# Performance work log

Hardware: AMD Instinct MI355X
Metric: run time of the kernel (lower is better)

## Reference

```python
import jax, jax.numpy as jnp
import numpy as np

B, C, F, T = 4, 64, 257, 256
H, OUT = 256, 64

def setup_inputs() -> dict:
    key = jax.random.key(0)
    ks = jax.random.split(key, 7)
    w = lambda k, shape: jax.random.normal(k, shape, dtype=jnp.float32) * 0.05
    return {
        "x": jax.random.normal(ks[0], (B, C, F, T), dtype=jnp.float32),
        "W_ih": w(ks[1], (4 * H, C)),   # torch LSTM weight_ih_l0, gate order i,f,g,o
        "W_hh": w(ks[2], (4 * H, H)),   # weight_hh_l0
        "b_ih": w(ks[3], (4 * H,)),
        "b_hh": w(ks[4], (4 * H,)),
        "W_lin": w(ks[5], (OUT, H)),
        "b_lin": w(ks[6], (OUT,)),
    }

def _lstm(y, W_ih, W_hh, b_ih, b_hh):
    # y: (N, T, C) -> (N, T, H); PyTorch gate order i, f, g, o
    N, Tl, _ = y.shape
    Hd = W_hh.shape[1]
    # precompute input contributions for all timesteps in one big GEMM
    x_gates = jnp.einsum('ntc,gc->ntg', y, W_ih) + b_ih + b_hh  # (N, T, 4H)

    def step(carry, xg):
        h, c = carry
        g = xg + h @ W_hh.T  # (N, 4H)
        i, f, gg, o = jnp.split(g, 4, axis=-1)
        c = jax.nn.sigmoid(f) * c + jax.nn.sigmoid(i) * jnp.tanh(gg)
        h = jax.nn.sigmoid(o) * jnp.tanh(c)
        return (h, c), h

    h0 = jnp.zeros((N, Hd), y.dtype)
    _, hs = jax.lax.scan(step, (h0, h0), jnp.swapaxes(x_gates, 0, 1))  # (T, N, H)
    return jnp.swapaxes(hs, 0, 1)  # (N, T, H)

def reference(x, W_ih, W_hh, b_ih, b_hh, W_lin, b_lin):
    b, c, f, t = x.shape
    y = x.transpose(0, 2, 3, 1).reshape(b * f, t, c)  # (B*F, T, C)
    h = _lstm(y, W_ih, W_hh, b_ih, b_hh)              # (B*F, T, H)
    out = h @ W_lin.T + b_lin                          # (B*F, T, OUT)
    return out.reshape(b, f, t, -1).transpose(0, 3, 1, 2)  # (B, OUT, F, T)
```

## Files before the change

kernel.cpp:

```cpp
#include <hip/hip_runtime.h>

#define NSEQ 1028
#define TT   256
#define CC   64
#define HH   256
#define NKT  10
#define AROWB 656
#define SLABE 32768
#define LSTM_LDS (2*16*AROWB + 2*SLABE*2)
#define OUTP_LDS (128*264*2 + 64*264*2)

typedef unsigned short u16;
typedef float  f32x4 __attribute__((ext_vector_type(4)));
typedef __bf16 v8bf  __attribute__((ext_vector_type(8)));

__device__ __forceinline__ u16 f2bf(float f){
  unsigned u = __builtin_bit_cast(unsigned, f);
  u += 0x7FFFu + ((u >> 16) & 1u);
  return (u16)(u >> 16);
}
__device__ __forceinline__ float sigm(float x){
  float t = __builtin_amdgcn_exp2f(-1.4426950408889634f * x);
  return __builtin_amdgcn_rcpf(1.0f + t);
}
__device__ __forceinline__ float tanh_f(float x){
  float a = __builtin_fabsf(x);
  float t = __builtin_amdgcn_exp2f(-2.885390081777927f * a);
  float r = (1.0f - t) * __builtin_amdgcn_rcpf(1.0f + t);
  return __builtin_copysignf(r, x);
}
__device__ __forceinline__ void mfma_a(f32x4& d, v8bf a, v8bf b){
  asm("v_mfma_f32_16x16x32_bf16 %0, %1, %2, %0" : "+v"(d) : "v"(a), "a"(b));
}
__device__ __forceinline__ void mfma_v(f32x4& d, v8bf a, v8bf b){
  asm("v_mfma_f32_16x16x32_bf16 %0, %1, %2, %0" : "+v"(d) : "v"(a), "v"(b));
}

__global__ void k_pack_w(const float* __restrict__ Whh, const float* __restrict__ Wih,
                         u16* __restrict__ wpack){
  int idx = blockIdx.x*256 + threadIdx.x;
  if (idx >= NKT*SLABE) return;
  int j    = idx & 7;
  int lane = (idx >> 3) & 63;
  int ct   = (idx >> 9) & 7;
  int w    = (idx >> 12) & 7;
  int kt   = idx >> 15;
  int col  = (ct >> 1)*256 + w*32 + (ct & 1)*16 + (lane & 15);
  int k    = kt*32 + (lane >> 4)*8 + j;
  float v  = (k < 256) ? Whh[col*256 + k] : Wih[col*64 + (k - 256)];
  wpack[idx] = f2bf(v);
}

__global__ void k_bias(const float* __restrict__ bi, const float* __restrict__ bh,
                       float* __restrict__ bias){
  int i = blockIdx.x*256 + threadIdx.x;
  if (i < 1024) bias[i] = bi[i] + bh[i];
}

__global__ void k_wlin(const float* __restrict__ Wl, u16* __restrict__ wlin){
  int i = blockIdx.x*256 + threadIdx.x;
  if (i >= 64*264) return;
  int col = i / 264, k = i % 264;
  wlin[i] = (k < 256) ? f2bf(Wl[col*256 + k]) : (u16)0;
}

__global__ void k_ytrans(const float* __restrict__ x, u16* __restrict__ ybuf){
  __shared__ u16 tile[64][257];
  int n = blockIdx.x, b = n / 257, f = n % 257, tid = threadIdx.x;
  for (int i = tid; i < 64*256; i += 256){
    int c = i >> 8, t = i & 255;
    tile[c][t] = f2bf(x[((size_t)(b*64 + c)*257 + f)*256 + t]);
  }
  __syncthreads();
  for (int i = tid; i < 256*64; i += 256){
    int t = i >> 6, c = i & 63;
    ybuf[((size_t)n*256 + t)*64 + c] = tile[c][t];
  }
}

__global__ __launch_bounds__(512, 2) void k_lstm(const u16* __restrict__ wpack,
      const float* __restrict__ bias, const u16* __restrict__ ybuf,
      u16* __restrict__ hbuf){
  extern __shared__ char smem[];
  char* lA = smem;
  u16*  lW = (u16*)(smem + 2*16*AROWB);
  const int tid = threadIdx.x, lane = tid & 63, w = tid >> 6;
  const int n0 = blockIdx.x * 16;
  const int l15 = lane & 15, q = lane >> 4;
  const int srow = tid >> 5, schunk = tid & 31;

  v8bf wreg[4][8];
  #pragma unroll
  for (int kt = 0; kt < 4; ++kt)
    #pragma unroll
    for (int ct = 0; ct < 8; ++ct)
      wreg[kt][ct] = *(const v8bf*)(wpack + ((kt*8 + w)*8 + ct)*512 + lane*8);

  {
    const uint4* src = (const uint4*)(wpack + 4*SLABE);
    uint4* dst = (uint4*)lW;
    for (int i = tid; i < (2*SLABE)/8; i += 512) dst[i] = src[i];
  }
  float biasr[8];
  #pragma unroll
  for (int ct = 0; ct < 8; ++ct)
    biasr[ct] = bias[(ct >> 1)*256 + w*32 + (ct & 1)*16 + l15];

  {
    unsigned* z = (unsigned*)lA;
    for (int i = tid; i < (2*16*AROWB)/4; i += 512) z[i] = 0;
  }
  __syncthreads();
  {
    unsigned v = 0;
    if (n0 + srow < NSEQ)
      v = *(const unsigned*)(ybuf + ((size_t)(n0 + srow)*TT + 0)*64 + schunk*2);
    *(unsigned*)(lA + srow*AROWB + 512 + schunk*4) = v;
  }
  f32x4 creg[2];
  creg[0] = (f32x4){0.f,0.f,0.f,0.f};
  creg[1] = (f32x4){0.f,0.f,0.f,0.f};
  __syncthreads();

  const u16* wp = wpack;

  v8bf sbuf[8];
  {
    const u16* wpw0 = wp + w*4096 + lane*8;
    #pragma unroll
    for (int ct = 0; ct < 8; ++ct) sbuf[ct] = *(const v8bf*)(wpw0 + 6*SLABE + ct*512);
  }

  for (int t = 0; t < TT; ++t){
    char* Acur = lA + (t & 1)*16*AROWB;
    char* Anxt = lA + ((t + 1) & 1)*16*AROWB;

    asm("" : "+s"(wp));
    const u16* wpw = wp + w*4096 + lane*8;

    unsigned yv = 0;
    if (t + 1 < TT && n0 + srow < NSEQ)
      yv = *(const unsigned*)(ybuf + ((size_t)(n0 + srow)*TT + (t + 1))*64 + schunk*2);

    if (t >= 1 && n0 + srow < NSEQ){
      uint4 hv = *(const uint4*)(Acur + srow*AROWB + schunk*16);
      *(uint4*)(hbuf + ((size_t)(n0 + srow)*TT + (t - 1))*HH + schunk*8) = hv;
    }

    f32x4 acc[8];
    #pragma unroll
    for (int ct = 0; ct < 8; ++ct)
      acc[ct] = (f32x4){biasr[ct], biasr[ct], biasr[ct], biasr[ct]};
    asm volatile("s_nop 1"
      : "+v"(acc[0]), "+v"(acc[1]), "+v"(acc[2]), "+v"(acc[3]),
        "+v"(acc[4]), "+v"(acc[5]), "+v"(acc[6]), "+v"(acc[7]));

    #define AFRAG(kt) (*(const v8bf*)(Acur + l15*AROWB + (kt)*64 + q*16))
    #define LFRAG(kt,ct) (*(const v8bf*)(lW + (((kt)-4)*8 + w)*4096 + (ct)*512 + lane*8))

    { v8bf a = AFRAG(0);
      #pragma unroll
      for (int ct = 0; ct < 8; ++ct) mfma_a(acc[ct], a, wreg[0][ct]); }
    { v8bf a = AFRAG(1);
      #pragma unroll
      for (int ct = 0; ct < 8; ++ct) mfma_a(acc[ct], a, wreg[1][ct]); }
    { v8bf a = AFRAG(6);
      #pragma unroll
      for (int ct = 0; ct < 8; ++ct) mfma_v(acc[ct], a, sbuf[ct]);
      #pragma unroll
      for (int ct = 0; ct < 8; ++ct) sbuf[ct] = *(const v8bf*)(wpw + 7*SLABE + ct*512);
      __builtin_amdgcn_sched_barrier(0); }
    { v8bf a = AFRAG(2);
      #pragma unroll
      for (int ct = 0; ct < 8; ++ct) mfma_a(acc[ct], a, wreg[2][ct]); }
    { v8bf a = AFRAG(3);
      #pragma unroll
      for (int ct = 0; ct < 8; ++ct) mfma_a(acc[ct], a, wreg[3][ct]); }
    { v8bf a = AFRAG(7);
      #pragma unroll
      for (int ct = 0; ct < 8; ++ct) mfma_v(acc[ct], a, sbuf[ct]);
      #pragma unroll
      for (int ct = 0; ct < 8; ++ct) sbuf[ct] = *(const v8bf*)(wpw + 8*SLABE + ct*512);
      __builtin_amdgcn_sched_barrier(0); }
    { v8bf a = AFRAG(4);
      #pragma unroll
      for (int ct = 0; ct < 8; ++ct) mfma_v(acc[ct], a, LFRAG(4,ct)); }
    { v8bf a = AFRAG(8);
      #pragma unroll
      for (int ct = 0; ct < 8; ++ct) mfma_v(acc[ct], a, sbuf[ct]);
      #pragma unroll
      for (int ct = 0; ct < 8; ++ct) sbuf[ct] = *(const v8bf*)(wpw + 9*SLABE + ct*512);
      __builtin_amdgcn_sched_barrier(0); }
    { v8bf a = AFRAG(5);
      #pragma unroll
      for (int ct = 0; ct < 8; ++ct) mfma_v(acc[ct], a, LFRAG(5,ct)); }
    { v8bf a = AFRAG(9);
      #pragma unroll
      for (int ct = 0; ct < 8; ++ct) mfma_v(acc[ct], a, sbuf[ct]);
      #pragma unroll
      for (int ct = 0; ct < 8; ++ct) sbuf[ct] = *(const v8bf*)(wpw + 6*SLABE + ct*512);
      __builtin_amdgcn_sched_barrier(0); }

    asm volatile("s_nop 7\n\ts_nop 7\n\ts_nop 7"
      : "+v"(acc[0]), "+v"(acc[1]), "+v"(acc[2]), "+v"(acc[3]),
        "+v"(acc[4]), "+v"(acc[5]), "+v"(acc[6]), "+v"(acc[7]));

    #pragma unroll
    for (int u = 0; u < 2; ++u){
      #pragma unroll
      for (int j = 0; j < 4; ++j){
        float xi = acc[0 + u][j], xf = acc[2 + u][j], xg = acc[4 + u][j], xo = acc[6 + u][j];
        float cv = sigm(xf)*creg[u][j] + sigm(xi)*tanh_f(xg);
        float hv = sigm(xo)*tanh_f(cv);
        creg[u][j] = cv;
        int row = 4*q + j, unit = w*32 + u*16 + l15;
        *(u16*)(Anxt + row*AROWB + unit*2) = f2bf(hv);
      }
    }
    if (t + 1 < TT)
      *(unsigned*)(Anxt + srow*AROWB + 512 + schunk*4) = yv;
    __syncthreads();
  }
  {
    char* Afin = lA + (TT & 1)*16*AROWB;
    if (n0 + srow < NSEQ){
      uint4 hv = *(const uint4*)(Afin + srow*AROWB + schunk*16);
      *(uint4*)(hbuf + ((size_t)(n0 + srow)*TT + (TT - 1))*HH + schunk*8) = hv;
    }
  }
}

__global__ __launch_bounds__(256) void k_outproj(const u16* __restrict__ hbuf,
      const u16* __restrict__ wlin, const float* __restrict__ blin,
      float* __restrict__ out){
  extern __shared__ char smem[];
  u16* sA = (u16*)smem;
  u16* sB = (u16*)(smem + 128*264*2);
  const int n = blockIdx.x, th = blockIdx.y, t0 = th*128;
  const int b = n / 257, f = n % 257;
  const int tid = threadIdx.x, lane = tid & 63, wv = tid >> 6;

  for (int i = tid; i < 128*32; i += 256){
    int r = i >> 5, part = i & 31;
    *(uint4*)(sA + r*264 + part*8) =
        *(const uint4*)(hbuf + ((size_t)n*TT + t0 + r)*HH + part*8);
  }
  for (int i = tid; i < (64*264)/2; i += 256)
    ((unsigned*)sB)[i] = ((const unsigned*)wlin)[i];
  __syncthreads();

  f32x4 acc[2][4];
  #pragma unroll
  for (int m = 0; m < 2; ++m)
    #pragma unroll
    for (int nt = 0; nt < 4; ++nt){
      float bv = blin[nt*16 + (lane & 15)];
      acc[m][nt] = (f32x4){bv, bv, bv, bv};
    }
  const int khi = (lane >> 4) * 8;
  #pragma unroll
  for (int kt = 0; kt < 8; ++kt){
    v8bf av[2];
    #pragma unroll
    for (int m = 0; m < 2; ++m){
      int mt = wv*2 + m;
      av[m] = *(const v8bf*)(sA + (mt*16 + (lane & 15))*264 + kt*32 + khi);
    }
    #pragma unroll
    for (int nt = 0; nt < 4; ++nt){
      v8bf bv = *(const v8bf*)(sB + (nt*16 + (lane & 15))*264 + kt*32 + khi);
      #pragma unroll
      for (int m = 0; m < 2; ++m)
        acc[m][nt] = __builtin_amdgcn_mfma_f32_16x16x32_bf16(av[m], bv, acc[m][nt], 0, 0, 0);
    }
  }
  #pragma unroll
  for (int m = 0; m < 2; ++m){
    int mt = wv*2 + m;
    #pragma unroll
    for (int nt = 0; nt < 4; ++nt){
      int o = nt*16 + (lane & 15);
      int tb = t0 + mt*16 + 4*(lane >> 4);
      *(f32x4*)(out + (((size_t)b*64 + o)*257 + f)*TT + tb) = acc[m][nt];
    }
  }
}

extern "C" void kernel_launch(void* const* d_in, const int* in_sizes, int n_in,
                              void* d_out, int out_size, void* d_ws, size_t ws_size,
                              hipStream_t stream) {
  const float* x   = (const float*)d_in[0];
  const float* Wih = (const float*)d_in[1];
  const float* Whh = (const float*)d_in[2];
  const float* bih = (const float*)d_in[3];
  const float* bhh = (const float*)d_in[4];
  const float* Wl  = (const float*)d_in[5];
  const float* bl  = (const float*)d_in[6];
  float* out = (float*)d_out;

  char* p = (char*)d_ws;
  u16*   wpack = (u16*)p;   p += 655360;
  float* bias  = (float*)p; p += 4096;
  u16*   wlin  = (u16*)p;   p += 33792;
  u16*   ybuf  = (u16*)p;   p += (size_t)NSEQ*TT*CC*2;
  u16*   hbuf  = (u16*)p;

  hipFuncSetAttribute((const void*)k_lstm,    hipFuncAttributeMaxDynamicSharedMemorySize, LSTM_LDS);
  hipFuncSetAttribute((const void*)k_outproj, hipFuncAttributeMaxDynamicSharedMemorySize, OUTP_LDS);

  k_pack_w <<<1280, 256, 0, stream>>>(Whh, Wih, wpack);
  k_bias   <<<4,    256, 0, stream>>>(bih, bhh, bias);
  k_wlin   <<<66,   256, 0, stream>>>(Wl, wlin);
  k_ytrans <<<1028, 256, 0, stream>>>(x, ybuf);
  k_lstm   <<<65, 512, LSTM_LDS, stream>>>(wpack, bias, ybuf, hbuf);
  k_outproj<<<dim3(1028, 2), 256, OUTP_LDS, stream>>>(hbuf, wlin, bl, out);
}
```

Measured before the change: 1.201 ms.

## Process 32 sequences per LSTM block, reusing each weight fragment across two M-tiles

```diff
diff --git a/kernel.cpp b/kernel.cpp
--- a/kernel.cpp
+++ b/kernel.cpp
@@ -6,8 +6,9 @@
 #define HH   256
 #define NKT  10
 #define AROWB 656
+#define A_BYTES (32*AROWB)
 #define SLABE 32768
-#define LSTM_LDS (2*16*AROWB + 2*SLABE*2)
+#define LSTM_LDS (A_BYTES + 2*SLABE*2)
 #define OUTP_LDS (128*264*2 + 64*264*2)
 
 typedef unsigned short u16;
@@ -83,21 +84,21 @@
       u16* __restrict__ hbuf){
   extern __shared__ char smem[];
   char* lA = smem;
-  u16*  lW = (u16*)(smem + 2*16*AROWB);
+  u16*  lW = (u16*)(smem + A_BYTES);
   const int tid = threadIdx.x, lane = tid & 63, w = tid >> 6;
-  const int n0 = blockIdx.x * 16;
+  const int n0 = blockIdx.x * 32;
   const int l15 = lane & 15, q = lane >> 4;
-  const int srow = tid >> 5, schunk = tid & 31;
-
-  v8bf wreg[4][8];
-  #pragma unroll
-  for (int kt = 0; kt < 4; ++kt)
+  const int yrow = tid >> 4, ychunk = tid & 15;
+
+  v8bf wreg[3][8];
+  #pragma unroll
+  for (int kt = 0; kt < 3; ++kt)
     #pragma unroll
     for (int ct = 0; ct < 8; ++ct)
       wreg[kt][ct] = *(const v8bf*)(wpack + ((kt*8 + w)*8 + ct)*512 + lane*8);
 
   {
-    const uint4* src = (const uint4*)(wpack + 4*SLABE);
+    const uint4* src = (const uint4*)(wpack + 3*SLABE);
     uint4* dst = (uint4*)lW;
     for (int i = tid; i < (2*SLABE)/8; i += 512) dst[i] = src[i];
   }
@@ -108,18 +109,18 @@
 
   {
     unsigned* z = (unsigned*)lA;
-    for (int i = tid; i < (2*16*AROWB)/4; i += 512) z[i] = 0;
+    for (int i = tid; i < A_BYTES/4; i += 512) z[i] = 0;
   }
   __syncthreads();
   {
-    unsigned v = 0;
-    if (n0 + srow < NSEQ)
-      v = *(const unsigned*)(ybuf + ((size_t)(n0 + srow)*TT + 0)*64 + schunk*2);
-    *(unsigned*)(lA + srow*AROWB + 512 + schunk*4) = v;
-  }
-  f32x4 creg[2];
-  creg[0] = (f32x4){0.f,0.f,0.f,0.f};
-  creg[1] = (f32x4){0.f,0.f,0.f,0.f};
+    uint2 v = {0u, 0u};
+    if (n0 + yrow < NSEQ)
+      v = *(const uint2*)(ybuf + ((size_t)(n0 + yrow)*TT + 0)*64 + ychunk*4);
+    *(uint2*)(lA + yrow*AROWB + 512 + ychunk*8) = v;
+  }
+  f32x4 creg[4];
+  #pragma unroll
+  for (int i = 0; i < 4; ++i) creg[i] = (f32x4){0.f,0.f,0.f,0.f};
   __syncthreads();
 
   const u16* wp = wpack;
@@ -128,105 +129,125 @@
   {
     const u16* wpw0 = wp + w*4096 + lane*8;
     #pragma unroll
-    for (int ct = 0; ct < 8; ++ct) sbuf[ct] = *(const v8bf*)(wpw0 + 6*SLABE + ct*512);
+    for (int ct = 0; ct < 8; ++ct) sbuf[ct] = *(const v8bf*)(wpw0 + 5*SLABE + ct*512);
   }
 
   for (int t = 0; t < TT; ++t){
-    char* Acur = lA + (t & 1)*16*AROWB;
-    char* Anxt = lA + ((t + 1) & 1)*16*AROWB;
-
     asm("" : "+s"(wp));
     const u16* wpw = wp + w*4096 + lane*8;
 
-    unsigned yv = 0;
-    if (t + 1 < TT && n0 + srow < NSEQ)
-      yv = *(const unsigned*)(ybuf + ((size_t)(n0 + srow)*TT + (t + 1))*64 + schunk*2);
-
-    if (t >= 1 && n0 + srow < NSEQ){
-      uint4 hv = *(const uint4*)(Acur + srow*AROWB + schunk*16);
-      *(uint4*)(hbuf + ((size_t)(n0 + srow)*TT + (t - 1))*HH + schunk*8) = hv;
-    }
-
-    f32x4 acc[8];
-    #pragma unroll
-    for (int ct = 0; ct < 8; ++ct)
-      acc[ct] = (f32x4){biasr[ct], biasr[ct], biasr[ct], biasr[ct]};
+    uint2 yv = {0u, 0u};
+    if (t + 1 < TT && n0 + yrow < NSEQ)
+      yv = *(const uint2*)(ybuf + ((size_t)(n0 + yrow)*TT + (t + 1))*64 + ychunk*4);
+
+    f32x4 acc[2][8];
+    #pragma unroll
+    for (int mt = 0; mt < 2; ++mt)
+      #pragma unroll
+      for (int ct = 0; ct < 8; ++ct)
+        acc[mt][ct] = (f32x4){biasr[ct], biasr[ct], biasr[ct], biasr[ct]};
     asm volatile("s_nop 1"
-      : "+v"(acc[0]), "+v"(acc[1]), "+v"(acc[2]), "+v"(acc[3]),
-        "+v"(acc[4]), "+v"(acc[5]), "+v"(acc[6]), "+v"(acc[7]));
-
-    #define AFRAG(kt) (*(const v8bf*)(Acur + l15*AROWB + (kt)*64 + q*16))
-    #define LFRAG(kt,ct) (*(const v8bf*)(lW + (((kt)-4)*8 + w)*4096 + (ct)*512 + lane*8))
-
-    { v8bf a = AFRAG(0);
-      #pragma unroll
-      for (int ct = 0; ct < 8; ++ct) mfma_a(acc[ct], a, wreg[0][ct]); }
-    { v8bf a = AFRAG(1);
-      #pragma unroll
-      for (int ct = 0; ct < 8; ++ct) mfma_a(acc[ct], a, wreg[1][ct]); }
-    { v8bf a = AFRAG(6);
-      #pragma unroll
-      for (int ct = 0; ct < 8; ++ct) mfma_v(acc[ct], a, sbuf[ct]);
+      : "+v"(acc[0][0]), "+v"(acc[0][1]), "+v"(acc[0][2]), "+v"(acc[0][3]),
+        "+v"(acc[0][4]), "+v"(acc[0][5]), "+v"(acc[0][6]), "+v"(acc[0][7]),
+        "+v"(acc[1][0]), "+v"(acc[1][1]), "+v"(acc[1][2]), "+v"(acc[1][3]),
+        "+v"(acc[1][4]), "+v"(acc[1][5]), "+v"(acc[1][6]), "+v"(acc[1][7]));
+
+    #define AFRAG(kt, mt) (*(const v8bf*)(lA + ((mt)*16 + l15)*AROWB + (kt)*64 + q*16))
+    #define LFRAG(kt, ct) (*(const v8bf*)(lW + (((kt)-3)*8 + w)*4096 + (ct)*512 + lane*8))
+
+    { v8bf a0 = AFRAG(0,0), a1 = AFRAG(0,1);
+      #pragma unroll
+      for (int ct = 0; ct < 8; ++ct){ mfma_a(acc[0][ct], a0, wreg[0][ct]);
+                                      mfma_a(acc[1][ct], a1, wreg[0][ct]); } }
+    { v8bf a0 = AFRAG(5,0), a1 = AFRAG(5,1);
+      #pragma unroll
+      for (int ct = 0; ct < 8; ++ct){ mfma_v(acc[0][ct], a0, sbuf[ct]);
+                                      mfma_v(acc[1][ct], a1, sbuf[ct]); }
+      #pragma unroll
+      for (int ct = 0; ct < 8; ++ct) sbuf[ct] = *(const v8bf*)(wpw + 6*SLABE + ct*512);
+      __builtin_amdgcn_sched_barrier(0); }
+    { v8bf a0 = AFRAG(1,0), a1 = AFRAG(1,1);
+      #pragma unroll
+      for (int ct = 0; ct < 8; ++ct){ mfma_a(acc[0][ct], a0, wreg[1][ct]);
+                                      mfma_a(acc[1][ct], a1, wreg[1][ct]); } }
+    { v8bf a0 = AFRAG(6,0), a1 = AFRAG(6,1);
+      #pragma unroll
+      for (int ct = 0; ct < 8; ++ct){ mfma_v(acc[0][ct], a0, sbuf[ct]);
+                                      mfma_v(acc[1][ct], a1, sbuf[ct]); }
       #pragma unroll
       for (int ct = 0; ct < 8; ++ct) sbuf[ct] = *(const v8bf*)(wpw + 7*SLABE + ct*512);
       __builtin_amdgcn_sched_barrier(0); }
-    { v8bf a = AFRAG(2);
-      #pragma unroll
-      for (int ct = 0; ct < 8; ++ct) mfma_a(acc[ct], a, wreg[2][ct]); }
-    { v8bf a = AFRAG(3);
-      #pragma unroll
-      for (int ct = 0; ct < 8; ++ct) mfma_a(acc[ct], a, wreg[3][ct]); }
-    { v8bf a = AFRAG(7);
-      #pragma unroll
-      for (int ct = 0; ct < 8; ++ct) mfma_v(acc[ct], a, sbuf[ct]);
+    { v8bf a0 = AFRAG(2,0), a1 = AFRAG(2,1);
+      #pragma unroll
+      for (int ct = 0; ct < 8; ++ct){ mfma_a(acc[0][ct], a0, wreg[2][ct]);
+                                      mfma_a(acc[1][ct], a1, wreg[2][ct]); } }
+    { v8bf a0 = AFRAG(7,0), a1 = AFRAG(7,1);
+      #pragma unroll
+      for (int ct = 0; ct < 8; ++ct){ mfma_v(acc[0][ct], a0, sbuf[ct]);
+                                      mfma_v(acc[1][ct], a1, sbuf[ct]); }
       #pragma unroll
       for (int ct = 0; ct < 8; ++ct) sbuf[ct] = *(const v8bf*)(wpw + 8*SLABE + ct*512);
       __builtin_amdgcn_sched_barrier(0); }
-    { v8bf a = AFRAG(4);
-      #pragma unroll
-      for (int ct = 0; ct < 8; ++ct) mfma_v(acc[ct], a, LFRAG(4,ct)); }
-    { v8bf a = AFRAG(8);
-      #pragma unroll
-      for (int ct = 0; ct < 8; ++ct) mfma_v(acc[ct], a, sbuf[ct]);
+    { v8bf a0 = AFRAG(3,0), a1 = AFRAG(3,1);
+      #pragma unroll
+      for (int ct = 0; ct < 8; ++ct){ v8bf b = LFRAG(3,ct);
+                                      mfma_v(acc[0][ct], a0, b);
+                                      mfma_v(acc[1][ct], a1, b); } }
+    { v8bf a0 = AFRAG(8,0), a1 = AFRAG(8,1);
+      #pragma unroll
+      for (int ct = 0; ct < 8; ++ct){ mfma_v(acc[0][ct], a0, sbuf[ct]);
+                                      mfma_v(acc[1][ct], a1, sbuf[ct]); }
       #pragma unroll
       for (int ct = 0; ct < 8; ++ct) sbuf[ct] = *(const v8bf*)(wpw + 9*SLABE + ct*512);
       __builtin_amdgcn_sched_barrier(0); }
-    { v8bf a = AFRAG(5);
-      #pragma unroll
-      for (int ct = 0; ct < 8; ++ct) mfma_v(acc[ct], a, LFRAG(5,ct)); }
-    { v8bf a = AFRAG(9);
-      #pragma unroll
-      for (int ct = 0; ct < 8; ++ct) mfma_v(acc[ct], a, sbuf[ct]);
-      #pragma unroll
-      for (int ct = 0; ct < 8; ++ct) sbuf[ct] = *(const v8bf*)(wpw + 6*SLABE + ct*512);
-      __builtin_amdgcn_sched_barrier(0); }
+    { v8bf a0 = AFRAG(4,0), a1 = AFRAG(4,1);
+      #pragma unroll
+      for (int ct = 0; ct < 8; ++ct){ v8bf b = LFRAG(4,ct);
+                                      mfma_v(acc[0][ct], a0, b);
+                                      mfma_v(acc[1][ct], a1, b); } }
+    { v8bf a0 = AFRAG(9,0), a1 = AFRAG(9,1);
+      #pragma unroll
+      for (int ct = 0; ct < 8; ++ct){ mfma_v(acc[0][ct], a0, sbuf[ct]);
+                                      mfma_v(acc[1][ct], a1, sbuf[ct]); } }
 
     asm volatile("s_nop 7\n\ts_nop 7\n\ts_nop 7"
-      : "+v"(acc[0]), "+v"(acc[1]), "+v"(acc[2]), "+v"(acc[3]),
-        "+v"(acc[4]), "+v"(acc[5]), "+v"(acc[6]), "+v"(acc[7]));
-
-    #pragma unroll
-    for (int u = 0; u < 2; ++u){
-      #pragma unroll
-      for (int j = 0; j < 4; ++j){
-        float xi = acc[0 + u][j], xf = acc[2 + u][j], xg = acc[4 + u][j], xo = acc[6 + u][j];
-        float cv = sigm(xf)*creg[u][j] + sigm(xi)*tanh_f(xg);
-        float hv = sigm(xo)*tanh_f(cv);
-        creg[u][j] = cv;
-        int row = 4*q + j, unit = w*32 + u*16 + l15;
-        *(u16*)(Anxt + row*AROWB + unit*2) = f2bf(hv);
+      : "+v"(acc[0][0]), "+v"(acc[0][1]), "+v"(acc[0][2]), "+v"(acc[0][3]),
+        "+v"(acc[0][4]), "+v"(acc[0][5]), "+v"(acc[0][6]), "+v"(acc[0][7]),
+        "+v"(acc[1][0]), "+v"(acc[1][1]), "+v"(acc[1][2]), "+v"(acc[1][3]),
+        "+v"(acc[1][4]), "+v"(acc[1][5]), "+v"(acc[1][6]), "+v"(acc[1][7]));
+
+    __syncthreads();
+
+    asm("" : "+s"(wp));
+    {
+      const u16* wpw2 = wp + w*4096 + lane*8;
+      #pragma unroll
+      for (int ct = 0; ct < 8; ++ct) sbuf[ct] = *(const v8bf*)(wpw2 + 5*SLABE + ct*512);
+      __builtin_amdgcn_sched_barrier(0);
+    }
+
+    #pragma unroll
+    for (int mt = 0; mt < 2; ++mt){
+      #pragma unroll
+      for (int u = 0; u < 2; ++u){
+        #pragma unroll
+        for (int j = 0; j < 4; ++j){
+          float xi = acc[mt][0 + u][j], xf = acc[mt][2 + u][j];
+          float xg = acc[mt][4 + u][j], xo = acc[mt][6 + u][j];
+          float cv = sigm(xf)*creg[mt*2 + u][j] + sigm(xi)*tanh_f(xg);
+          float hv = sigm(xo)*tanh_f(cv);
+          creg[mt*2 + u][j] = cv;
+          int row = mt*16 + 4*q + j, colu = w*32 + u*16 + l15;
+          u16 hb = f2bf(hv);
+          *(u16*)(lA + row*AROWB + colu*2) = hb;
+          if (n0 + row < NSEQ)
+            hbuf[((size_t)(n0 + row)*TT + t)*HH + colu] = hb;
+        }
       }
     }
     if (t + 1 < TT)
-      *(unsigned*)(Anxt + srow*AROWB + 512 + schunk*4) = yv;
+      *(uint2*)(lA + yrow*AROWB + 512 + ychunk*8) = yv;
     __syncthreads();
-  }
-  {
-    char* Afin = lA + (TT & 1)*16*AROWB;
-    if (n0 + srow < NSEQ){
-      uint4 hv = *(const uint4*)(Afin + srow*AROWB + schunk*16);
-      *(uint4*)(hbuf + ((size_t)(n0 + srow)*TT + (TT - 1))*HH + schunk*8) = hv;
-    }
   }
 }
 
@@ -312,6 +333,6 @@
   k_bias   <<<4,    256, 0, stream>>>(bih, bhh, bias);
   k_wlin   <<<66,   256, 0, stream>>>(Wl, wlin);
   k_ytrans <<<1028, 256, 0, stream>>>(x, ybuf);
-  k_lstm   <<<65, 512, LSTM_LDS, stream>>>(wpack, bias, ybuf, hbuf);
+  k_lstm   <<<33, 512, LSTM_LDS, stream>>>(wpack, bias, ybuf, hbuf);
   k_outproj<<<dim3(1028, 2), 256, OUTP_LDS, stream>>>(hbuf, wlin, bl, out);
 }
```

Result: slower. 2.062 ms (+71.6%).

## Precompute input-gate contributions in a parallel kernel before the LSTM recurrence

Applied to the files above, without the earlier changes.

```diff
diff --git a/kernel.cpp b/kernel.cpp
--- a/kernel.cpp
+++ b/kernel.cpp
@@ -4,10 +4,12 @@
 #define TT   256
 #define CC   64
 #define HH   256
-#define NKT  10
+#define SLABE 32768
+#define AROWX 528
+#define XG_A  (16*AROWX)
+#define XG_LDS (2*XG_A + 2*SLABE*2)
 #define AROWB 656
-#define SLABE 32768
-#define LSTM_LDS (2*16*AROWB + 2*SLABE*2)
+#define FB_LDS (2*16*AROWB + 2*SLABE*2)
 #define OUTP_LDS (128*264*2 + 64*264*2)
 
 typedef unsigned short u16;
@@ -39,7 +41,7 @@
 __global__ void k_pack_w(const float* __restrict__ Whh, const float* __restrict__ Wih,
                          u16* __restrict__ wpack){
   int idx = blockIdx.x*256 + threadIdx.x;
-  if (idx >= NKT*SLABE) return;
+  if (idx >= 10*SLABE) return;
   int j    = idx & 7;
   int lane = (idx >> 3) & 63;
   int ct   = (idx >> 9) & 7;
@@ -78,7 +80,204 @@
   }
 }
 
-__global__ __launch_bounds__(512, 2) void k_lstm(const u16* __restrict__ wpack,
+__global__ __launch_bounds__(512) void k_xgates(const u16* __restrict__ wpack,
+      const float* __restrict__ bias, const u16* __restrict__ ybuf,
+      u16* __restrict__ xgp){
+  __shared__ u16 yt[16*16*72];
+  const int g = blockIdx.x, t0 = blockIdx.y*16, n0 = g*16;
+  const int tid = threadIdx.x, lane = tid & 63, w = tid >> 6;
+  const int l15 = lane & 15, q = lane >> 4;
+
+  v8bf wf[2][8];
+  #pragma unroll
+  for (int kf = 0; kf < 2; ++kf)
+    #pragma unroll
+    for (int ct = 0; ct < 8; ++ct)
+      wf[kf][ct] = *(const v8bf*)(wpack + (((8 + kf)*8 + w)*8 + ct)*512 + lane*8);
+  float biasr[8];
+  #pragma unroll
+  for (int ct = 0; ct < 8; ++ct)
+    biasr[ct] = bias[(ct >> 1)*256 + w*32 + (ct & 1)*16 + l15];
+
+  #pragma unroll
+  for (int s = 0; s < 4; ++s){
+    int i = tid + s*512;
+    int seq = i >> 7, tt = (i >> 3) & 15, c8 = i & 7;
+    uint4 v = {0u,0u,0u,0u};
+    if (n0 + seq < NSEQ)
+      v = *(const uint4*)(ybuf + ((size_t)(n0 + seq)*TT + t0 + tt)*64 + c8*8);
+    *(uint4*)(yt + tt*1152 + seq*72 + c8*8) = v;
+  }
+  __syncthreads();
+
+  for (int tt = 0; tt < 16; ++tt){
+    f32x4 acc[8];
+    #pragma unroll
+    for (int ct = 0; ct < 8; ++ct)
+      acc[ct] = (f32x4){biasr[ct], biasr[ct], biasr[ct], biasr[ct]};
+    v8bf a0 = *(const v8bf*)(yt + tt*1152 + l15*72 + q*8);
+    v8bf a1 = *(const v8bf*)(yt + tt*1152 + l15*72 + 32 + q*8);
+    #pragma unroll
+    for (int ct = 0; ct < 8; ++ct){
+      acc[ct] = __builtin_amdgcn_mfma_f32_16x16x32_bf16(a0, wf[0][ct], acc[ct], 0, 0, 0);
+      acc[ct] = __builtin_amdgcn_mfma_f32_16x16x32_bf16(a1, wf[1][ct], acc[ct], 0, 0, 0);
+    }
+    unsigned dw[16];
+    #pragma unroll
+    for (int ct = 0; ct < 8; ++ct)
+      #pragma unroll
+      for (int p = 0; p < 2; ++p)
+        dw[ct*2 + p] = (unsigned)f2bf(acc[ct][2*p]) | ((unsigned)f2bf(acc[ct][2*p + 1]) << 16);
+    u16* dst = xgp + ((((size_t)g*TT + t0 + tt)*8 + w)*64 + lane)*32;
+    *(uint4*)(dst +  0) = (uint4){dw[0], dw[1], dw[2], dw[3]};
+    *(uint4*)(dst +  8) = (uint4){dw[4], dw[5], dw[6], dw[7]};
+    *(uint4*)(dst + 16) = (uint4){dw[8], dw[9], dw[10], dw[11]};
+    *(uint4*)(dst + 24) = (uint4){dw[12], dw[13], dw[14], dw[15]};
+  }
+}
+
+__global__ __launch_bounds__(512, 2) void k_lstm_xg(const u16* __restrict__ wpack,
+      const u16* __restrict__ xgp, u16* __restrict__ hbuf){
+  extern __shared__ char smem[];
+  char* lA = smem;
+  u16*  lW = (u16*)(smem + 2*XG_A);
+  const int tid = threadIdx.x, lane = tid & 63, w = tid >> 6;
+  const int g = blockIdx.x, n0 = g*16;
+  const int l15 = lane & 15, q = lane >> 4;
+  const int srow = tid >> 5, schunk = tid & 31;
+
+  v8bf wreg[4][8];
+  #pragma unroll
+  for (int kt = 0; kt < 4; ++kt)
+    #pragma unroll
+    for (int ct = 0; ct < 8; ++ct)
+      wreg[kt][ct] = *(const v8bf*)(wpack + ((kt*8 + w)*8 + ct)*512 + lane*8);
+
+  {
+    const uint4* src = (const uint4*)(wpack + 4*SLABE);
+    uint4* dst = (uint4*)lW;
+    for (int i = tid; i < (2*SLABE)/8; i += 512) dst[i] = src[i];
+  }
+  {
+    unsigned* z = (unsigned*)lA;
+    for (int i = tid; i < (2*XG_A)/4; i += 512) z[i] = 0;
+  }
+  f32x4 creg[2];
+  creg[0] = (f32x4){0.f,0.f,0.f,0.f};
+  creg[1] = (f32x4){0.f,0.f,0.f,0.f};
+  __syncthreads();
+
+  const u16* wp = wpack;
+
+  v8bf sbuf[8];
+  uint4 xgv[4];
+  {
+    const u16* wpw0 = wp + w*4096 + lane*8;
+    #pragma unroll
+    for (int ct = 0; ct < 8; ++ct) sbuf[ct] = *(const v8bf*)(wpw0 + 6*SLABE + ct*512);
+    const u16* xb = xgp + ((((size_t)g*TT + 0)*8 + w)*64 + lane)*32;
+    xgv[0] = *(const uint4*)(xb +  0);
+    xgv[1] = *(const uint4*)(xb +  8);
+    xgv[2] = *(const uint4*)(xb + 16);
+    xgv[3] = *(const uint4*)(xb + 24);
+  }
+
+  for (int t = 0; t < TT; ++t){
+    char* Acur = lA + (t & 1)*XG_A;
+    char* Anxt = lA + ((t + 1) & 1)*XG_A;
+    asm("" : "+s"(wp));
+    const u16* wpw = wp + w*4096 + lane*8;
+
+    if (t >= 1 && n0 + srow < NSEQ){
+      uint4 hv = *(const uint4*)(Acur + srow*AROWX + schunk*16);
+      *(uint4*)(hbuf + ((size_t)(n0 + srow)*TT + (t - 1))*HH + schunk*8) = hv;
+    }
+
+    f32x4 acc[8];
+    #pragma unroll
+    for (int ct = 0; ct < 8; ++ct){
+      #pragma unroll
+      for (int p = 0; p < 2; ++p){
+        unsigned u = ((const unsigned*)&xgv[(ct*2 + p) >> 2])[(ct*2 + p) & 3];
+        acc[ct][2*p]     = __builtin_bit_cast(float, u << 16);
+        acc[ct][2*p + 1] = __builtin_bit_cast(float, u & 0xffff0000u);
+      }
+    }
+    asm volatile("s_nop 1"
+      : "+v"(acc[0]), "+v"(acc[1]), "+v"(acc[2]), "+v"(acc[3]),
+        "+v"(acc[4]), "+v"(acc[5]), "+v"(acc[6]), "+v"(acc[7]));
+
+    if (t + 1 < TT){
+      const u16* xb = xgp + ((((size_t)g*TT + (t + 1))*8 + w)*64 + lane)*32;
+      xgv[0] = *(const uint4*)(xb +  0);
+      xgv[1] = *(const uint4*)(xb +  8);
+      xgv[2] = *(const uint4*)(xb + 16);
+      xgv[3] = *(const uint4*)(xb + 24);
+    }
+    __builtin_amdgcn_sched_barrier(0);
+
+    #define AFRAGX(kt) (*(const v8bf*)(Acur + l15*AROWX + (kt)*64 + q*16))
+    #define LFRAGX(kt,ct) (*(const v8bf*)(lW + (((kt)-4)*8 + w)*4096 + (ct)*512 + lane*8))
+
+    { v8bf a = AFRAGX(0);
+      #pragma unroll
+      for (int ct = 0; ct < 8; ++ct) mfma_a(acc[ct], a, wreg[0][ct]); }
+    { v8bf a = AFRAGX(6);
+      #pragma unroll
+      for (int ct = 0; ct < 8; ++ct) mfma_v(acc[ct], a, sbuf[ct]);
+      #pragma unroll
+      for (int ct = 0; ct < 8; ++ct) sbuf[ct] = *(const v8bf*)(wpw + 7*SLABE + ct*512);
+      __builtin_amdgcn_sched_barrier(0); }
+    { v8bf a = AFRAGX(1);
+      #pragma unroll
+      for (int ct = 0; ct < 8; ++ct) mfma_a(acc[ct], a, wreg[1][ct]); }
+    { v8bf a = AFRAGX(2);
+      #pragma unroll
+      for (int ct = 0; ct < 8; ++ct) mfma_a(acc[ct], a, wreg[2][ct]); }
+    { v8bf a = AFRAGX(3);
+      #pragma unroll
+      for (int ct = 0; ct < 8; ++ct) mfma_a(acc[ct], a, wreg[3][ct]); }
+    { v8bf a = AFRAGX(4);
+      #pragma unroll
+      for (int ct = 0; ct < 8; ++ct) mfma_v(acc[ct], a, LFRAGX(4,ct)); }
+    { v8bf a = AFRAGX(7);
+      #pragma unroll
+      for (int ct = 0; ct < 8; ++ct) mfma_v(acc[ct], a, sbuf[ct]);
+      #pragma unroll
+      for (int ct = 0; ct < 8; ++ct) sbuf[ct] = *(const v8bf*)(wpw + 6*SLABE + ct*512);
+      __builtin_amdgcn_sched_barrier(0); }
+    { v8bf a = AFRAGX(5);
+      #pragma unroll
+      for (int ct = 0; ct < 8; ++ct) mfma_v(acc[ct], a, LFRAGX(5,ct)); }
+
+    asm volatile("s_nop 7\n\ts_nop 7\n\ts_nop 7"
+      : "+v"(acc[0]), "+v"(acc[1]), "+v"(acc[2]), "+v"(acc[3]),
+        "+v"(acc[4]), "+v"(acc[5]), "+v"(acc[6]), "+v"(acc[7]));
+
+    #pragma unroll
+    for (int u = 0; u < 2; ++u){
+      #pragma unroll
+      for (int j = 0; j < 4; ++j){
+        float xi = acc[0 + u][j], xf = acc[2 + u][j], xg = acc[4 + u][j], xo = acc[6 + u][j];
+        float cv = sigm(xf)*creg[u][j] + sigm(xi)*tanh_f(xg);
+        float hv = sigm(xo)*tanh_f(cv);
+        creg[u][j] = cv;
+        int row = 4*q + j, unit = w*32 + u*16 + l15;
+        *(u16*)(Anxt + row*AROWX + unit*2) = f2bf(hv);
+      }
+    }
+    __syncthreads();
+  }
+  {
+    char* Afin = lA + (TT & 1)*XG_A;
+    if (n0 + srow < NSEQ){
+      uint4 hv = *(const uint4*)(Afin + srow*AROWX + schunk*16);
+      *(uint4*)(hbuf + ((size_t)(n0 + srow)*TT + (TT - 1))*HH + schunk*8) = hv;
+    }
+  }
+}
+
+__global__ __launch_bounds__(512, 2) void k_lstm_fb(const u16* __restrict__ wpack,
       const float* __restrict__ bias, const u16* __restrict__ ybuf,
       u16* __restrict__ hbuf){
   extern __shared__ char smem[];
@@ -95,7 +294,6 @@
     #pragma unroll
     for (int ct = 0; ct < 8; ++ct)
       wreg[kt][ct] = *(const v8bf*)(wpack + ((kt*8 + w)*8 + ct)*512 + lane*8);
-
   {
     const uint4* src = (const uint4*)(wpack + 4*SLABE);
     uint4* dst = (uint4*)lW;
@@ -105,7 +303,6 @@
   #pragma unroll
   for (int ct = 0; ct < 8; ++ct)
     biasr[ct] = bias[(ct >> 1)*256 + w*32 + (ct & 1)*16 + l15];
-
   {
     unsigned* z = (unsigned*)lA;
     for (int i = tid; i < (2*16*AROWB)/4; i += 512) z[i] = 0;
@@ -114,8 +311,8 @@
   {
     unsigned v = 0;
     if (n0 + srow < NSEQ)
-      v = *(const unsigned*)(ybuf + ((size_t)(n0 + srow)*TT + 0)*64 + schunk*2);
-    *(unsigned*)(lA + srow*AROWB + 512 + schunk*4) = v;
+      v = *(const unsigned*)(ybuf + ((size_t)(n0 + srow)*TT + 0)*64 + (tid & 31)*2);
+    *(unsigned*)(lA + srow*AROWB + 512 + (tid & 31)*4) = v;
   }
   f32x4 creg[2];
   creg[0] = (f32x4){0.f,0.f,0.f,0.f};
@@ -123,7 +320,6 @@
   __syncthreads();
 
   const u16* wp = wpack;
-
   v8bf sbuf[8];
   {
     const u16* wpw0 = wp + w*4096 + lane*8;
@@ -134,13 +330,12 @@
   for (int t = 0; t < TT; ++t){
     char* Acur = lA + (t & 1)*16*AROWB;
     char* Anxt = lA + ((t + 1) & 1)*16*AROWB;
-
     asm("" : "+s"(wp));
     const u16* wpw = wp + w*4096 + lane*8;
 
     unsigned yv = 0;
     if (t + 1 < TT && n0 + srow < NSEQ)
-      yv = *(const unsigned*)(ybuf + ((size_t)(n0 + srow)*TT + (t + 1))*64 + schunk*2);
+      yv = *(const unsigned*)(ybuf + ((size_t)(n0 + srow)*TT + (t + 1))*64 + (tid & 31)*2);
 
     if (t >= 1 && n0 + srow < NSEQ){
       uint4 hv = *(const uint4*)(Acur + srow*AROWB + schunk*16);
@@ -218,7 +413,7 @@
       }
     }
     if (t + 1 < TT)
-      *(unsigned*)(Anxt + srow*AROWB + 512 + schunk*4) = yv;
+      *(unsigned*)(Anxt + srow*AROWB + 512 + (tid & 31)*4) = yv;
     __syncthreads();
   }
   {
@@ -303,15 +498,25 @@
   float* bias  = (float*)p; p += 4096;
   u16*   wlin  = (u16*)p;   p += 33792;
   u16*   ybuf  = (u16*)p;   p += (size_t)NSEQ*TT*CC*2;
-  u16*   hbuf  = (u16*)p;
-
-  hipFuncSetAttribute((const void*)k_lstm,    hipFuncAttributeMaxDynamicSharedMemorySize, LSTM_LDS);
+  u16*   hbuf  = (u16*)p;   p += (size_t)NSEQ*TT*HH*2;
+  u16*   xgp   = (u16*)p;
+  const size_t XGP_BYTES = (size_t)65*TT*8*64*32*2;
+  const size_t NEED = (size_t)(p - (char*)d_ws) + XGP_BYTES;
+
+  hipFuncSetAttribute((const void*)k_lstm_xg, hipFuncAttributeMaxDynamicSharedMemorySize, XG_LDS);
+  hipFuncSetAttribute((const void*)k_lstm_fb, hipFuncAttributeMaxDynamicSharedMemorySize, FB_LDS);
   hipFuncSetAttribute((const void*)k_outproj, hipFuncAttributeMaxDynamicSharedMemorySize, OUTP_LDS);
 
   k_pack_w <<<1280, 256, 0, stream>>>(Whh, Wih, wpack);
   k_bias   <<<4,    256, 0, stream>>>(bih, bhh, bias);
   k_wlin   <<<66,   256, 0, stream>>>(Wl, wlin);
   k_ytrans <<<1028, 256, 0, stream>>>(x, ybuf);
-  k_lstm   <<<65, 512, LSTM_LDS, stream>>>(wpack, bias, ybuf, hbuf);
+
+  if (ws_size >= NEED) {
+    k_xgates <<<dim3(65, 16), 512, 0, stream>>>(wpack, bias, ybuf, xgp);
+    k_lstm_xg<<<65, 512, XG_LDS, stream>>>(wpack, xgp, hbuf);
+  } else {
+    k_lstm_fb<<<65, 512, FB_LDS, stream>>>(wpack, bias, ybuf, hbuf);
+  }
   k_outproj<<<dim3(1028, 2), 256, OUTP_LDS, stream>>>(hbuf, wlin, bl, out);
 }
```

New measurement: 1.199 ms. No clear change (-0.2%).
